# Kernel optimization log

Measured on AMD Instinct MI355X. Metric: run time of the kernel, lower is better.

## Reference

```python
import math
import jax, jax.numpy as jnp
import numpy as np

DIM_IN = 2048
DIM_OUT = 2048
BLOCK = 128
N_BLOCKS = 256
SPARSITY = 0.1
BATCH = 8192


def setup_inputs() -> dict:
    key = jax.random.key(0)
    k1, k2, k3, k4, k5 = jax.random.split(key, 5)
    x = jax.random.normal(k1, (BATCH, DIM_IN), dtype=jnp.float32)
    weight = jax.random.normal(k2, (DIM_IN, DIM_OUT), dtype=jnp.float32) * (1.0 / math.sqrt(DIM_IN))
    bias = jax.random.normal(k3, (DIM_OUT,), dtype=jnp.float32) * 0.01
    gate_w = jax.random.normal(k4, (DIM_IN, N_BLOCKS), dtype=jnp.float32) * (1.0 / math.sqrt(DIM_IN))
    gate_b = jax.random.normal(k5, (N_BLOCKS,), dtype=jnp.float32) * 0.01
    return {"x": x, "weight": weight, "bias": bias, "gate_w": gate_w, "gate_b": gate_b}


def _sparsify1d(g):
    # k-th largest kept per row; threshold, mask, renormalize (Sparsify1D)
    n = g.shape[-1]
    k = int(math.ceil(SPARSITY * n))
    topval = jax.lax.top_k(g, k)[0][:, -1:]          # (B, 1) k-th largest value
    res = jnp.where(g >= topval, g, jnp.zeros_like(g))
    return res / (jnp.sum(res, axis=-1, keepdims=True) / n)


def reference(x, weight, bias, gate_w, gate_b):
    B = x.shape[0]
    s = DIM_IN // BLOCK                               # 16 block-rows/cols
    # gate network: Linear -> Sparsify1D
    g = _sparsify1d(x @ gate_w + gate_b)              # (B, s*s)
    gb = g.reshape(B, s, s)                           # (B, s_in, s_out)
    xb = x.reshape(B, s, BLOCK)                       # (B, s_in, block)
    Wb = weight.reshape(s, BLOCK, s, BLOCK)           # (s_in, block, s_out, block)
    # gated block matrix-vector multiply:
    # y[b,q,n] = sum_{p,m} g[b,p,q] * x[b,p,m] * W[p,m,q,n]
    y = jnp.einsum('bpq,bpm,pmqn->bqn', gb, xb, Wb)
    return y.reshape(B, DIM_OUT) + bias
```

## Files before the change

### kernel.cpp

```cpp
#include <hip/hip_runtime.h>
#include <hip/hip_bf16.h>
#include <stdint.h>

#define BATCH  8192
#define DIN    2048
#define DOUT   2048
#define NB     256
#define KSEL   26
#define GDELTA 1e-4f

typedef __attribute__((ext_vector_type(2))) float f32x2;
typedef __attribute__((ext_vector_type(4))) float f32x4;
typedef __attribute__((ext_vector_type(16))) float f32x16;
typedef __attribute__((ext_vector_type(8))) __bf16 bf16x8;
typedef __attribute__((ext_vector_type(8))) unsigned short u16x8;
typedef __attribute__((ext_vector_type(4))) unsigned short u16x4;

__device__ __forceinline__ float bf2f(unsigned short u){
  union { unsigned int i; float f; } v; v.i = ((unsigned int)u) << 16; return v.f;
}
__device__ __forceinline__ unsigned short f2bf(float f){
  union { float f; unsigned int i; } v; v.f = f;
  unsigned int x = v.i;
  return (unsigned short)((x + 0x7FFFu + ((x >> 16) & 1u)) >> 16);
}
__device__ __forceinline__ unsigned short f2bf_c(float f){
  __bf16 b = (__bf16)f;
  union { __bf16 b; unsigned short u; } v; v.b = b; return v.u;
}

__global__ __launch_bounds__(256) void conv_wt(const float* __restrict__ w, unsigned short* __restrict__ wt)
{
  __shared__ float tl[64][65];
  const int k0 = blockIdx.x * 64;
  const int n0 = blockIdx.y * 64;
  const int c  = threadIdx.x & 63;
  const int r4 = threadIdx.x >> 6;
  #pragma unroll
  for (int i = 0; i < 16; i++){
    const int r = r4 * 16 + i;
    tl[r][c] = w[(size_t)(k0 + r) * DOUT + n0 + c];
  }
  __syncthreads();
  #pragma unroll
  for (int i = 0; i < 16; i++){
    const int n = r4 * 16 + i;
    wt[(size_t)(n0 + n) * DIN + k0 + c] = f2bf(tl[c][n]);
  }
}

__global__ __launch_bounds__(256) void conv_gwt(const float* __restrict__ gw,
    unsigned short* __restrict__ ghiT, unsigned short* __restrict__ gloT)
{
  __shared__ float tl[64][65];
  const int k0 = blockIdx.x * 64;
  const int n0 = blockIdx.y * 64;
  const int c  = threadIdx.x & 63;
  const int r4 = threadIdx.x >> 6;
  #pragma unroll
  for (int i = 0; i < 16; i++){
    const int r = r4 * 16 + i;
    tl[r][c] = gw[(size_t)(k0 + r) * NB + n0 + c];
  }
  __syncthreads();
  #pragma unroll
  for (int i = 0; i < 16; i++){
    const int n = r4 * 16 + i;
    const float v = tl[c][n];
    const unsigned short h = f2bf_c(v);
    ghiT[(size_t)(n0 + n) * DIN + k0 + c] = h;
    gloT[(size_t)(n0 + n) * DIN + k0 + c] = f2bf_c(v - bf2f(h));
  }
}

__global__ __launch_bounds__(256) void gate_mfma(
    const float* __restrict__ x,
    const unsigned short* __restrict__ ghiT,
    const unsigned short* __restrict__ gloT,
    float* __restrict__ part,
    unsigned short* __restrict__ xb)
{
  __shared__ unsigned short Ah[2][32][40], Al[2][32][40];
  __shared__ unsigned short Bh[2][256][40], Bl[2][256][40];

  const int b0   = blockIdx.x * 32;
  const int t    = threadIdx.x;
  const int lane = t & 63;
  const int wv   = t >> 6;
  const int l31  = lane & 31;
  const int lk   = (lane >> 5) * 8;

  const int sr = t >> 3;
  const int sk = (t & 7) * 4;
  const int bc = t >> 2;
  const int bk = (t & 3) * 8;

  f32x16 acc[2];
  acc[0] = (f32x16)0.f; acc[1] = (f32x16)0.f;

  auto STAGE = [&](int bb, int k0){
    f32x4 a = *(const f32x4*)&x[(size_t)(b0 + sr) * DIN + k0 + sk];
    u16x4 hi4, lo4;
    #pragma unroll
    for (int j = 0; j < 4; j++){
      const unsigned short h = f2bf_c(a[j]);
      hi4[j] = h;
      lo4[j] = f2bf_c(a[j] - bf2f(h));
    }
    *(u16x4*)&Ah[bb][sr][sk] = hi4;
    *(u16x4*)&Al[bb][sr][sk] = lo4;
    *(u16x4*)&xb[(size_t)(b0 + sr) * DIN + k0 + sk] = hi4;
    #pragma unroll
    for (int p = 0; p < 4; p++){
      const int col = bc + p * 64;
      u16x8 vh = *(const u16x8*)&ghiT[(size_t)col * DIN + k0 + bk];
      *(u16x8*)&Bh[bb][col][bk] = vh;
      u16x8 vl = *(const u16x8*)&gloT[(size_t)col * DIN + k0 + bk];
      *(u16x8*)&Bl[bb][col][bk] = vl;
    }
  };

  STAGE(0, 0);
  __syncthreads();
  int cur = 0;
  for (int ks = 0; ks < 64; ks++){
    if (ks < 63) STAGE(cur ^ 1, (ks + 1) * 32);
    bf16x8 ah[2], al[2], bh[2][2], bl[2][2];
    #pragma unroll
    for (int kh = 0; kh < 2; kh++){
      const int ko = kh * 16 + lk;
      ah[kh] = *(const bf16x8*)&Ah[cur][l31][ko];
      al[kh] = *(const bf16x8*)&Al[cur][l31][ko];
      #pragma unroll
      for (int n = 0; n < 2; n++){
        bh[n][kh] = *(const bf16x8*)&Bh[cur][wv * 64 + n * 32 + l31][ko];
        bl[n][kh] = *(const bf16x8*)&Bl[cur][wv * 64 + n * 32 + l31][ko];
      }
    }
    #pragma unroll
    for (int n = 0; n < 2; n++)
      #pragma unroll
      for (int kh = 0; kh < 2; kh++){
        acc[n] = __builtin_amdgcn_mfma_f32_32x32x16_bf16(ah[kh], bh[n][kh], acc[n], 0, 0, 0);
        acc[n] = __builtin_amdgcn_mfma_f32_32x32x16_bf16(ah[kh], bl[n][kh], acc[n], 0, 0, 0);
        acc[n] = __builtin_amdgcn_mfma_f32_32x32x16_bf16(al[kh], bh[n][kh], acc[n], 0, 0, 0);
      }
    __syncthreads();
    cur ^= 1;
  }

  #pragma unroll
  for (int n = 0; n < 2; n++){
    const int col = wv * 64 + n * 32 + l31;
    #pragma unroll
    for (int r = 0; r < 16; r++){
      const int row = (r & 3) + 8 * (r >> 2) + 4 * (lane >> 5);
      part[(size_t)(b0 + row) * NB + col] = acc[n][r];
    }
  }
}

__global__ __launch_bounds__(256) void topk(float* __restrict__ part,
    const float* __restrict__ gb, int* __restrict__ flags)
{
  const int lane = threadIdx.x & 63;
  const int row  = blockIdx.x * 4 + (threadIdx.x >> 6);
  f32x4* p0 = (f32x4*)&part[(size_t)row * NB];
  const f32x4* gbv = (const f32x4*)gb;
  f32x4 v = p0[lane] + gbv[lane];

  const float NEG = -3.402823466e38f;
  float w0 = v[0], w1 = v[1], w2 = v[2], w3 = v[3];
  float thr = 0.f, nxt = 0.f;
  for (int it = 0; it < KSEL + 1; it++){
    float lm = fmaxf(fmaxf(w0, w1), fmaxf(w2, w3));
    float wm = lm;
    #pragma unroll
    for (int off = 32; off; off >>= 1) wm = fmaxf(wm, __shfl_xor(wm, off, 64));
    unsigned long long ball = __ballot(lm == wm);
    int first = __ffsll(ball) - 1;
    if (lane == first){
      if      (w0 == wm) w0 = NEG;
      else if (w1 == wm) w1 = NEG;
      else if (w2 == wm) w2 = NEG;
      else               w3 = NEG;
    }
    if (it < KSEL) thr = wm; else nxt = wm;
  }
  if (lane == 0) flags[row] = (thr - nxt < GDELTA) ? 1 : 0;

  float s = 0.f;
  #pragma unroll
  for (int j = 0; j < 4; j++) s += (v[j] >= thr) ? v[j] : 0.f;
  #pragma unroll
  for (int off = 32; off; off >>= 1) s += __shfl_xor(s, off, 64);
  const float d = s * (1.0f / NB);
  f32x4 o;
  #pragma unroll
  for (int j = 0; j < 4; j++) o[j] = (v[j] >= thr) ? v[j] / d : 0.f;
  p0[lane] = o;
}

__global__ __launch_bounds__(256) void refine(
    const float* __restrict__ x, const float* __restrict__ gw,
    const float* __restrict__ gb, const int* __restrict__ flags,
    float* __restrict__ part)
{
  const int lane = threadIdx.x & 63;
  const int row  = blockIdx.x * 4 + (threadIdx.x >> 6);
  if (!flags[row]) return;

  f32x4 acc0 = (f32x4)0.f, acc1 = (f32x4)0.f;
  const float* xp = &x[(size_t)row * DIN];
  #pragma unroll 8
  for (int k = 0; k < 1024; k++){
    const float xv = xp[k];
    const f32x4 wv = *(const f32x4*)&gw[(size_t)k * NB + lane * 4];
    #pragma unroll
    for (int j = 0; j < 4; j++) acc0[j] = fmaf(xv, wv[j], acc0[j]);
  }
  #pragma unroll 8
  for (int k = 1024; k < 2048; k++){
    const float xv = xp[k];
    const f32x4 wv = *(const f32x4*)&gw[(size_t)k * NB + lane * 4];
    #pragma unroll
    for (int j = 0; j < 4; j++) acc1[j] = fmaf(xv, wv[j], acc1[j]);
  }
  const f32x4 gbv = *(const f32x4*)&gb[lane * 4];
  f32x4 v;
  #pragma unroll
  for (int j = 0; j < 4; j++) v[j] = acc0[j] + acc1[j] + gbv[j];

  const float NEG = -3.402823466e38f;
  float w0 = v[0], w1 = v[1], w2 = v[2], w3 = v[3];
  float thr = 0.f;
  for (int it = 0; it < KSEL; it++){
    float lm = fmaxf(fmaxf(w0, w1), fmaxf(w2, w3));
    float wm = lm;
    #pragma unroll
    for (int off = 32; off; off >>= 1) wm = fmaxf(wm, __shfl_xor(wm, off, 64));
    unsigned long long ball = __ballot(lm == wm);
    int first = __ffsll(ball) - 1;
    if (lane == first){
      if      (w0 == wm) w0 = NEG;
      else if (w1 == wm) w1 = NEG;
      else if (w2 == wm) w2 = NEG;
      else               w3 = NEG;
    }
    thr = wm;
  }
  float s = 0.f;
  #pragma unroll
  for (int j = 0; j < 4; j++) s += (v[j] >= thr) ? v[j] : 0.f;
  #pragma unroll
  for (int off = 32; off; off >>= 1) s += __shfl_xor(s, off, 64);
  const float d = s * (1.0f / NB);
  f32x4 o;
  #pragma unroll
  for (int j = 0; j < 4; j++) o[j] = (v[j] >= thr) ? v[j] / d : 0.f;
  *(f32x4*)&part[(size_t)row * NB + lane * 4] = o;
}

__global__ __launch_bounds__(256) void main_gemm(
    const unsigned short* __restrict__ xb,
    const unsigned short* __restrict__ wt,
    const float* __restrict__ g,
    const float* __restrict__ bias,
    float* __restrict__ out)
{
  __shared__ unsigned short xa[128][72];
  __shared__ unsigned short wb[128][72];
  __shared__ float gl[128 * 17];

  const int q    = blockIdx.x;
  const int b0   = blockIdx.y * 128;
  const int t    = threadIdx.x;
  const int lane = t & 63;
  const int wid  = t >> 6;
  const int wr   = (wid >> 1) * 64;
  const int wc   = (wid & 1) * 64;
  const int l15  = lane & 15;
  const int l4   = lane >> 4;

  for (int e = t; e < 128 * 16; e += 256){
    const int r = e >> 4, p = e & 15;
    gl[r * 17 + p] = g[(size_t)(b0 + r) * NB + p * 16 + q];
  }

  f32x4 acc[4][4];
  #pragma unroll
  for (int m = 0; m < 4; m++)
    #pragma unroll
    for (int n = 0; n < 4; n++) acc[m][n] = (f32x4)0.0f;

  const int row_s = t >> 1;
  const int half  = t & 1;

  for (int kp = 0; kp < 32; kp++){
    const int p = kp >> 1;
    __syncthreads();
    {
      const float gate = gl[row_s * 17 + p];
      const unsigned short* src = &xb[(size_t)(b0 + row_s) * DIN + kp * 64 + half * 32];
      unsigned short* dst = &xa[row_s][half * 32];
      #pragma unroll
      for (int c = 0; c < 4; c++){
        u16x8 u = *(const u16x8*)(src + c * 8);
        u16x8 o;
        #pragma unroll
        for (int j = 0; j < 8; j++) o[j] = f2bf_c(bf2f(u[j]) * gate);
        *(u16x8*)(dst + c * 8) = o;
      }
    }
    {
      const unsigned short* src = &wt[(size_t)(q * 128 + row_s) * DIN + kp * 64 + half * 32];
      unsigned short* dst = &wb[row_s][half * 32];
      #pragma unroll
      for (int c = 0; c < 4; c++)
        *(u16x8*)(dst + c * 8) = *(const u16x8*)(src + c * 8);
    }
    __syncthreads();
    #pragma unroll
    for (int ksi = 0; ksi < 2; ksi++){
      const int kk = ksi * 32 + l4 * 8;
      bf16x8 a[4], b[4];
      #pragma unroll
      for (int m = 0; m < 4; m++)
        a[m] = *(const bf16x8*)&xa[wr + m * 16 + l15][kk];
      #pragma unroll
      for (int n = 0; n < 4; n++)
        b[n] = *(const bf16x8*)&wb[wc + n * 16 + l15][kk];
      #pragma unroll
      for (int m = 0; m < 4; m++)
        #pragma unroll
        for (int n = 0; n < 4; n++)
          acc[m][n] = __builtin_amdgcn_mfma_f32_16x16x32_bf16(a[m], b[n], acc[m][n], 0, 0, 0);
    }
  }

  #pragma unroll
  for (int n = 0; n < 4; n++){
    const int col = q * 128 + wc + n * 16 + l15;
    const float bv = bias[col];
    #pragma unroll
    for (int m = 0; m < 4; m++){
      #pragma unroll
      for (int r = 0; r < 4; r++){
        const int row = b0 + wr + m * 16 + l4 * 4 + r;
        out[(size_t)row * DOUT + col] = acc[m][n][r] + bv;
      }
    }
  }
}

extern "C" void kernel_launch(void* const* d_in, const int* in_sizes, int n_in,
                              void* d_out, int out_size, void* d_ws, size_t ws_size,
                              hipStream_t stream)
{
  const float* x    = (const float*)d_in[0];
  const float* w    = (const float*)d_in[1];
  const float* bias = (const float*)d_in[2];
  const float* gw   = (const float*)d_in[3];
  const float* gb   = (const float*)d_in[4];
  float* out = (float*)d_out;

  char* wsb = (char*)d_ws;
  float*          part = (float*)wsb;
  unsigned short* wtb  = (unsigned short*)(wsb + (size_t)8  * 1024 * 1024);
  unsigned short* xbb  = (unsigned short*)(wsb + (size_t)16 * 1024 * 1024);
  unsigned short* ghiT = (unsigned short*)(wsb + (size_t)48 * 1024 * 1024);
  unsigned short* gloT = (unsigned short*)(wsb + (size_t)49 * 1024 * 1024);
  int*            flg  = (int*)           (wsb + (size_t)50 * 1024 * 1024);

  conv_wt  <<<dim3(DIN / 64, DOUT / 64), 256, 0, stream>>>(w, wtb);
  conv_gwt <<<dim3(DIN / 64, NB / 64),   256, 0, stream>>>(gw, ghiT, gloT);
  gate_mfma<<<BATCH / 32, 256, 0, stream>>>(x, ghiT, gloT, part, xbb);
  topk     <<<BATCH / 4, 256, 0, stream>>>(part, gb, flg);
  refine   <<<BATCH / 4, 256, 0, stream>>>(x, gw, gb, flg, part);
  main_gemm<<<dim3(16, BATCH / 128), 256, 0, stream>>>(xbb, wtb, part, bias, out);
}
```

Measured before the change: 305.5 us.

## Restructure gate GEMM with split-K, transposed tiling and register-loaded x

Rewrites the gate GEMM so that gate weights become the LDS-staged A operand and x is loaded straight into registers and split into hi/lo bf16 there. The reduction over K is split four ways across grid z, and topk sums the four partial results. The bf16 copy of x is no longer written, so main_gemm reads fp32 x and converts it after gating. This aims for more parallelism and less LDS and global traffic in the gate stage, at the cost of extra partial-buffer writes and the main GEMM reading twice as many bytes of x. Scaling fp32 x by the gate before rounding also changes the numerics slightly.

```diff
diff --git a/kernel.cpp b/kernel.cpp
--- a/kernel.cpp
+++ b/kernel.cpp
@@ -73,91 +73,117 @@
   }
 }
 
-__global__ __launch_bounds__(256) void gate_mfma(
+__global__ __launch_bounds__(256) void gate_flip(
     const float* __restrict__ x,
     const unsigned short* __restrict__ ghiT,
     const unsigned short* __restrict__ gloT,
-    float* __restrict__ part,
-    unsigned short* __restrict__ xb)
-{
-  __shared__ unsigned short Ah[2][32][40], Al[2][32][40];
-  __shared__ unsigned short Bh[2][256][40], Bl[2][256][40];
-
-  const int b0   = blockIdx.x * 32;
+    float* __restrict__ part)
+{
+  __shared__ unsigned short Ah[2][64][40], Al[2][64][40];
+
+  const int c0   = blockIdx.x * 64;
+  const int b0   = blockIdx.y * 256;
+  const int ks   = blockIdx.z;
+  const int k0   = ks * 512;
   const int t    = threadIdx.x;
   const int lane = t & 63;
   const int wv   = t >> 6;
   const int l31  = lane & 31;
   const int lk   = (lane >> 5) * 8;
 
-  const int sr = t >> 3;
-  const int sk = (t & 7) * 4;
-  const int bc = t >> 2;
-  const int bk = (t & 3) * 8;
-
-  f32x16 acc[2];
-  acc[0] = (f32x16)0.f; acc[1] = (f32x16)0.f;
-
-  auto STAGE = [&](int bb, int k0){
-    f32x4 a = *(const f32x4*)&x[(size_t)(b0 + sr) * DIN + k0 + sk];
-    u16x4 hi4, lo4;
-    #pragma unroll
-    for (int j = 0; j < 4; j++){
-      const unsigned short h = f2bf_c(a[j]);
-      hi4[j] = h;
-      lo4[j] = f2bf_c(a[j] - bf2f(h));
-    }
-    *(u16x4*)&Ah[bb][sr][sk] = hi4;
-    *(u16x4*)&Al[bb][sr][sk] = lo4;
-    *(u16x4*)&xb[(size_t)(b0 + sr) * DIN + k0 + sk] = hi4;
-    #pragma unroll
-    for (int p = 0; p < 4; p++){
-      const int col = bc + p * 64;
-      u16x8 vh = *(const u16x8*)&ghiT[(size_t)col * DIN + k0 + bk];
-      *(u16x8*)&Bh[bb][col][bk] = vh;
-      u16x8 vl = *(const u16x8*)&gloT[(size_t)col * DIN + k0 + bk];
-      *(u16x8*)&Bl[bb][col][bk] = vl;
-    }
+  const int sc = t >> 2;
+  const int sk = (t & 3) * 8;
+
+  f32x16 acc[2][2];
+  #pragma unroll
+  for (int m = 0; m < 2; m++)
+    #pragma unroll
+    for (int n = 0; n < 2; n++) acc[m][n] = (f32x16)0.f;
+
+  auto STAGE = [&](int bb, int kc){
+    *(u16x8*)&Ah[bb][sc][sk] = *(const u16x8*)&ghiT[(size_t)(c0 + sc) * DIN + kc + sk];
+    *(u16x8*)&Al[bb][sc][sk] = *(const u16x8*)&gloT[(size_t)(c0 + sc) * DIN + kc + sk];
   };
 
-  STAGE(0, 0);
-  __syncthreads();
-  int cur = 0;
-  for (int ks = 0; ks < 64; ks++){
-    if (ks < 63) STAGE(cur ^ 1, (ks + 1) * 32);
-    bf16x8 ah[2], al[2], bh[2][2], bl[2][2];
+  auto LOADB = [&](f32x4 (&xr)[2][2][2], int kc){
+    #pragma unroll
+    for (int n = 0; n < 2; n++){
+      const size_t rowb = (size_t)(b0 + wv * 64 + n * 32 + l31) * DIN;
+      #pragma unroll
+      for (int kh = 0; kh < 2; kh++){
+        const float* xp = &x[rowb + kc + kh * 16 + lk];
+        xr[n][kh][0] = *(const f32x4*)xp;
+        xr[n][kh][1] = *(const f32x4*)(xp + 4);
+      }
+    }
+  };
+
+  auto COMP = [&](const f32x4 (&xr)[2][2][2], int bb){
+    bf16x8 bhf[2][2], blf[2][2];
+    #pragma unroll
+    for (int n = 0; n < 2; n++)
+      #pragma unroll
+      for (int kh = 0; kh < 2; kh++){
+        bf16x8 h, l;
+        #pragma unroll
+        for (int q = 0; q < 2; q++)
+          #pragma unroll
+          for (int j = 0; j < 4; j++){
+            const float v = xr[n][kh][q][j];
+            const __bf16 hb = (__bf16)v;
+            h[q * 4 + j] = hb;
+            l[q * 4 + j] = (__bf16)(v - (float)hb);
+          }
+        bhf[n][kh] = h; blf[n][kh] = l;
+      }
     #pragma unroll
     for (int kh = 0; kh < 2; kh++){
       const int ko = kh * 16 + lk;
-      ah[kh] = *(const bf16x8*)&Ah[cur][l31][ko];
-      al[kh] = *(const bf16x8*)&Al[cur][l31][ko];
-      #pragma unroll
-      for (int n = 0; n < 2; n++){
-        bh[n][kh] = *(const bf16x8*)&Bh[cur][wv * 64 + n * 32 + l31][ko];
-        bl[n][kh] = *(const bf16x8*)&Bl[cur][wv * 64 + n * 32 + l31][ko];
-      }
-    }
-    #pragma unroll
-    for (int n = 0; n < 2; n++)
-      #pragma unroll
-      for (int kh = 0; kh < 2; kh++){
-        acc[n] = __builtin_amdgcn_mfma_f32_32x32x16_bf16(ah[kh], bh[n][kh], acc[n], 0, 0, 0);
-        acc[n] = __builtin_amdgcn_mfma_f32_32x32x16_bf16(ah[kh], bl[n][kh], acc[n], 0, 0, 0);
-        acc[n] = __builtin_amdgcn_mfma_f32_32x32x16_bf16(al[kh], bh[n][kh], acc[n], 0, 0, 0);
-      }
+      #pragma unroll
+      for (int m = 0; m < 2; m++){
+        const bf16x8 ah = *(const bf16x8*)&Ah[bb][m * 32 + l31][ko];
+        const bf16x8 al = *(const bf16x8*)&Al[bb][m * 32 + l31][ko];
+        #pragma unroll
+        for (int n = 0; n < 2; n++){
+          acc[m][n] = __builtin_amdgcn_mfma_f32_32x32x16_bf16(ah, bhf[n][kh], acc[m][n], 0, 0, 0);
+          acc[m][n] = __builtin_amdgcn_mfma_f32_32x32x16_bf16(al, bhf[n][kh], acc[m][n], 0, 0, 0);
+          acc[m][n] = __builtin_amdgcn_mfma_f32_32x32x16_bf16(ah, blf[n][kh], acc[m][n], 0, 0, 0);
+        }
+      }
+    }
+  };
+
+  f32x4 xrA[2][2][2], xrB[2][2][2];
+  LOADB(xrA, k0);
+  STAGE(0, k0);
+  __syncthreads();
+  #pragma unroll 1
+  for (int it = 0; it < 8; it++){
+    const int kc = k0 + it * 64;
+    LOADB(xrB, kc + 32);
+    STAGE(1, kc + 32);
+    COMP(xrA, 0);
     __syncthreads();
-    cur ^= 1;
-  }
-
-  #pragma unroll
-  for (int n = 0; n < 2; n++){
-    const int col = wv * 64 + n * 32 + l31;
-    #pragma unroll
-    for (int r = 0; r < 16; r++){
-      const int row = (r & 3) + 8 * (r >> 2) + 4 * (lane >> 5);
-      part[(size_t)(b0 + row) * NB + col] = acc[n][r];
-    }
-  }
+    if (it < 7){
+      LOADB(xrA, kc + 64);
+      STAGE(0, kc + 64);
+    }
+    COMP(xrB, 1);
+    __syncthreads();
+  }
+
+  float* dst = part + (size_t)ks * BATCH * NB;
+  #pragma unroll
+  for (int m = 0; m < 2; m++)
+    #pragma unroll
+    for (int n = 0; n < 2; n++){
+      const int brow = b0 + wv * 64 + n * 32 + l31;
+      #pragma unroll
+      for (int r = 0; r < 16; r++){
+        const int ccol = c0 + m * 32 + (r & 3) + 8 * (r >> 2) + 4 * (lane >> 5);
+        dst[(size_t)brow * NB + ccol] = acc[m][n][r];
+      }
+    }
 }
 
 __global__ __launch_bounds__(256) void topk(float* __restrict__ part,
@@ -166,8 +192,11 @@
   const int lane = threadIdx.x & 63;
   const int row  = blockIdx.x * 4 + (threadIdx.x >> 6);
   f32x4* p0 = (f32x4*)&part[(size_t)row * NB];
+  const f32x4* p1 = (const f32x4*)&part[(size_t)(BATCH + row) * NB];
+  const f32x4* p2 = (const f32x4*)&part[(size_t)(2 * BATCH + row) * NB];
+  const f32x4* p3 = (const f32x4*)&part[(size_t)(3 * BATCH + row) * NB];
   const f32x4* gbv = (const f32x4*)gb;
-  f32x4 v = p0[lane] + gbv[lane];
+  f32x4 v = ((p0[lane] + p1[lane]) + p2[lane]) + p3[lane] + gbv[lane];
 
   const float NEG = -3.402823466e38f;
   float w0 = v[0], w1 = v[1], w2 = v[2], w3 = v[3];
@@ -262,7 +291,7 @@
 }
 
 __global__ __launch_bounds__(256) void main_gemm(
-    const unsigned short* __restrict__ xb,
+    const float* __restrict__ x,
     const unsigned short* __restrict__ wt,
     const float* __restrict__ g,
     const float* __restrict__ bias,
@@ -301,14 +330,18 @@
     __syncthreads();
     {
       const float gate = gl[row_s * 17 + p];
-      const unsigned short* src = &xb[(size_t)(b0 + row_s) * DIN + kp * 64 + half * 32];
+      const float* src = &x[(size_t)(b0 + row_s) * DIN + kp * 64 + half * 32];
       unsigned short* dst = &xa[row_s][half * 32];
       #pragma unroll
       for (int c = 0; c < 4; c++){
-        u16x8 u = *(const u16x8*)(src + c * 8);
+        f32x4 a0 = *(const f32x4*)(src + c * 8);
+        f32x4 a1 = *(const f32x4*)(src + c * 8 + 4);
         u16x8 o;
         #pragma unroll
-        for (int j = 0; j < 8; j++) o[j] = f2bf_c(bf2f(u[j]) * gate);
+        for (int j = 0; j < 4; j++){
+          o[j]     = f2bf_c(a0[j] * gate);
+          o[4 + j] = f2bf_c(a1[j] * gate);
+        }
         *(u16x8*)(dst + c * 8) = o;
       }
     }
@@ -366,16 +399,15 @@
 
   char* wsb = (char*)d_ws;
   float*          part = (float*)wsb;
-  unsigned short* wtb  = (unsigned short*)(wsb + (size_t)8  * 1024 * 1024);
-  unsigned short* xbb  = (unsigned short*)(wsb + (size_t)16 * 1024 * 1024);
-  unsigned short* ghiT = (unsigned short*)(wsb + (size_t)48 * 1024 * 1024);
-  unsigned short* gloT = (unsigned short*)(wsb + (size_t)49 * 1024 * 1024);
-  int*            flg  = (int*)           (wsb + (size_t)50 * 1024 * 1024);
+  unsigned short* wtb  = (unsigned short*)(wsb + (size_t)32 * 1024 * 1024);
+  unsigned short* ghiT = (unsigned short*)(wsb + (size_t)40 * 1024 * 1024);
+  unsigned short* gloT = (unsigned short*)(wsb + (size_t)41 * 1024 * 1024);
+  int*            flg  = (int*)           (wsb + (size_t)42 * 1024 * 1024);
 
   conv_wt  <<<dim3(DIN / 64, DOUT / 64), 256, 0, stream>>>(w, wtb);
   conv_gwt <<<dim3(DIN / 64, NB / 64),   256, 0, stream>>>(gw, ghiT, gloT);
-  gate_mfma<<<BATCH / 32, 256, 0, stream>>>(x, ghiT, gloT, part, xbb);
+  gate_flip<<<dim3(NB / 64, BATCH / 256, 4), 256, 0, stream>>>(x, ghiT, gloT, part);
   topk     <<<BATCH / 4, 256, 0, stream>>>(part, gb, flg);
   refine   <<<BATCH / 4, 256, 0, stream>>>(x, gw, gb, flg, part);
-  main_gemm<<<dim3(16, BATCH / 128), 256, 0, stream>>>(xbb, wtb, part, bias, out);
-}
+  main_gemm<<<dim3(16, BATCH / 128), 256, 0, stream>>>(x, wtb, part, bias, out);
+}
```

After: 343.1 us. 1.12x slower.

## Split-K gate GEMM, swizzled LDS, register prefetch, and reorder main GEMM blocks

Applied to the files above, without the earlier changes.

The gate GEMM is rewritten to use 64x128 tiles with 16x16x32 MFMAs, XOR-swizzled unpadded LDS, and a split-K over two halves. It writes two partial sums that topk now adds together. The main GEMM also gets swizzled LDS, global-to-register prefetch of the next K slice that overlaps the MFMA work, and a flattened 1D grid with a remapped batch order. The weight conversion moves after refine so its buffer can reuse the gate-weight workspace. The intent is to cut LDS bank conflicts and exposed load latency and to raise gate parallelism, at the cost of extra partial-sum traffic and a tighter workspace overlap.

```diff
diff --git a/kernel.cpp b/kernel.cpp
--- a/kernel.cpp
+++ b/kernel.cpp
@@ -73,89 +73,143 @@
   }
 }
 
-__global__ __launch_bounds__(256) void gate_mfma(
+__global__ __launch_bounds__(256) void gate_v2(
     const float* __restrict__ x,
     const unsigned short* __restrict__ ghiT,
     const unsigned short* __restrict__ gloT,
     float* __restrict__ part,
     unsigned short* __restrict__ xb)
 {
-  __shared__ unsigned short Ah[2][32][40], Al[2][32][40];
-  __shared__ unsigned short Bh[2][256][40], Bl[2][256][40];
-
-  const int b0   = blockIdx.x * 32;
+  __shared__ unsigned short Axh[64][64], Axl[64][64];
+  __shared__ unsigned short Bgh[128][64], Bgl[128][64];
+
+  const int b0   = blockIdx.x * 64;
+  const int c0   = blockIdx.y * 128;
+  const int ks   = blockIdx.z;
+  const int k0   = ks * 1024;
   const int t    = threadIdx.x;
   const int lane = t & 63;
   const int wv   = t >> 6;
-  const int l31  = lane & 31;
-  const int lk   = (lane >> 5) * 8;
-
-  const int sr = t >> 3;
-  const int sk = (t & 7) * 4;
-  const int bc = t >> 2;
-  const int bk = (t & 3) * 8;
-
-  f32x16 acc[2];
-  acc[0] = (f32x16)0.f; acc[1] = (f32x16)0.f;
-
-  auto STAGE = [&](int bb, int k0){
-    f32x4 a = *(const f32x4*)&x[(size_t)(b0 + sr) * DIN + k0 + sk];
-    u16x4 hi4, lo4;
+  const int bw   = wv & 1;
+  const int cw   = wv >> 1;
+  const int l15  = lane & 15;
+  const int l4   = lane >> 4;
+  const bool emit = (blockIdx.y == 0);
+
+  const int ar = t >> 2;
+  const int ak = (t & 3) * 16;
+  const int br = t >> 1;
+  const int bk = (t & 1) * 32;
+
+  f32x4 acc[2][4];
+  #pragma unroll
+  for (int m = 0; m < 2; m++)
+    #pragma unroll
+    for (int n = 0; n < 4; n++) acc[m][n] = (f32x4)0.0f;
+
+  int aoff[2][2], boff[2][4];
+  #pragma unroll
+  for (int ksi = 0; ksi < 2; ksi++){
+    const int chunk = ksi * 4 + l4;
+    #pragma unroll
+    for (int m = 0; m < 2; m++){
+      const int row = bw * 32 + m * 16 + l15;
+      aoff[ksi][m] = row * 64 + ((chunk ^ (row & 7)) << 3);
+    }
+    #pragma unroll
+    for (int n = 0; n < 4; n++){
+      const int row = cw * 64 + n * 16 + l15;
+      boff[ksi][n] = row * 64 + ((chunk ^ (row & 7)) << 3);
+    }
+  }
+
+  f32x4 xa[4];
+  u16x8 gh[4], glo[4];
+
+  auto LOAD = [&](int kb){
+    const float* xp = &x[(size_t)(b0 + ar) * DIN + kb + ak];
+    #pragma unroll
+    for (int j = 0; j < 4; j++) xa[j] = ((const f32x4*)xp)[j];
+    const unsigned short* hp = &ghiT[(size_t)(c0 + br) * DIN + kb + bk];
+    const unsigned short* lp = &gloT[(size_t)(c0 + br) * DIN + kb + bk];
+    #pragma unroll
+    for (int j = 0; j < 4; j++){ gh[j] = ((const u16x8*)hp)[j]; glo[j] = ((const u16x8*)lp)[j]; }
+  };
+
+  auto WRITE = [&](int kb){
+    const int asw = ar & 7;
+    #pragma unroll
+    for (int h = 0; h < 2; h++){
+      u16x8 hi, lo;
+      #pragma unroll
+      for (int j = 0; j < 8; j++){
+        const float v = xa[h * 2 + (j >> 2)][j & 3];
+        const __bf16 hb = (__bf16)v;
+        union { __bf16 b; unsigned short u; } uh; uh.b = hb;
+        hi[j] = uh.u;
+        lo[j] = f2bf_c(v - (float)hb);
+      }
+      const int c8 = (((ak >> 3) + h) ^ asw) << 3;
+      *(u16x8*)&Axh[ar][c8] = hi;
+      *(u16x8*)&Axl[ar][c8] = lo;
+      if (emit) *(u16x8*)&xb[(size_t)(b0 + ar) * DIN + kb + ak + h * 8] = hi;
+    }
+    const int bsw = br & 7;
     #pragma unroll
     for (int j = 0; j < 4; j++){
-      const unsigned short h = f2bf_c(a[j]);
-      hi4[j] = h;
-      lo4[j] = f2bf_c(a[j] - bf2f(h));
-    }
-    *(u16x4*)&Ah[bb][sr][sk] = hi4;
-    *(u16x4*)&Al[bb][sr][sk] = lo4;
-    *(u16x4*)&xb[(size_t)(b0 + sr) * DIN + k0 + sk] = hi4;
-    #pragma unroll
-    for (int p = 0; p < 4; p++){
-      const int col = bc + p * 64;
-      u16x8 vh = *(const u16x8*)&ghiT[(size_t)col * DIN + k0 + bk];
-      *(u16x8*)&Bh[bb][col][bk] = vh;
-      u16x8 vl = *(const u16x8*)&gloT[(size_t)col * DIN + k0 + bk];
-      *(u16x8*)&Bl[bb][col][bk] = vl;
+      const int c8 = (((bk >> 3) + j) ^ bsw) << 3;
+      *(u16x8*)&Bgh[br][c8] = gh[j];
+      *(u16x8*)&Bgl[br][c8] = glo[j];
     }
   };
 
-  STAGE(0, 0);
-  __syncthreads();
-  int cur = 0;
-  for (int ks = 0; ks < 64; ks++){
-    if (ks < 63) STAGE(cur ^ 1, (ks + 1) * 32);
-    bf16x8 ah[2], al[2], bh[2][2], bl[2][2];
-    #pragma unroll
-    for (int kh = 0; kh < 2; kh++){
-      const int ko = kh * 16 + lk;
-      ah[kh] = *(const bf16x8*)&Ah[cur][l31][ko];
-      al[kh] = *(const bf16x8*)&Al[cur][l31][ko];
-      #pragma unroll
-      for (int n = 0; n < 2; n++){
-        bh[n][kh] = *(const bf16x8*)&Bh[cur][wv * 64 + n * 32 + l31][ko];
-        bl[n][kh] = *(const bf16x8*)&Bl[cur][wv * 64 + n * 32 + l31][ko];
+  const unsigned short* Ah0 = &Axh[0][0];
+  const unsigned short* Al0 = &Axl[0][0];
+  const unsigned short* Bh0 = &Bgh[0][0];
+  const unsigned short* Bl0 = &Bgl[0][0];
+
+  LOAD(k0);
+  #pragma unroll 1
+  for (int s = 0; s < 16; s++){
+    const int kb = k0 + s * 64;
+    __syncthreads();
+    WRITE(kb);
+    __syncthreads();
+    if (s < 15) LOAD(kb + 64);
+    #pragma unroll
+    for (int ksi = 0; ksi < 2; ksi++){
+      bf16x8 ah[2], al[2], bh[4], bl[4];
+      #pragma unroll
+      for (int m = 0; m < 2; m++){
+        ah[m] = *(const bf16x8*)&Ah0[aoff[ksi][m]];
+        al[m] = *(const bf16x8*)&Al0[aoff[ksi][m]];
       }
-    }
-    #pragma unroll
-    for (int n = 0; n < 2; n++)
-      #pragma unroll
-      for (int kh = 0; kh < 2; kh++){
-        acc[n] = __builtin_amdgcn_mfma_f32_32x32x16_bf16(ah[kh], bh[n][kh], acc[n], 0, 0, 0);
-        acc[n] = __builtin_amdgcn_mfma_f32_32x32x16_bf16(ah[kh], bl[n][kh], acc[n], 0, 0, 0);
-        acc[n] = __builtin_amdgcn_mfma_f32_32x32x16_bf16(al[kh], bh[n][kh], acc[n], 0, 0, 0);
+      #pragma unroll
+      for (int n = 0; n < 4; n++){
+        bh[n] = *(const bf16x8*)&Bh0[boff[ksi][n]];
+        bl[n] = *(const bf16x8*)&Bl0[boff[ksi][n]];
       }
-    __syncthreads();
-    cur ^= 1;
-  }
-
-  #pragma unroll
-  for (int n = 0; n < 2; n++){
-    const int col = wv * 64 + n * 32 + l31;
-    #pragma unroll
-    for (int r = 0; r < 16; r++){
-      const int row = (r & 3) + 8 * (r >> 2) + 4 * (lane >> 5);
-      part[(size_t)(b0 + row) * NB + col] = acc[n][r];
+      #pragma unroll
+      for (int m = 0; m < 2; m++)
+        #pragma unroll
+        for (int n = 0; n < 4; n++){
+          acc[m][n] = __builtin_amdgcn_mfma_f32_16x16x32_bf16(ah[m], bh[n], acc[m][n], 0, 0, 0);
+          acc[m][n] = __builtin_amdgcn_mfma_f32_16x16x32_bf16(al[m], bh[n], acc[m][n], 0, 0, 0);
+          acc[m][n] = __builtin_amdgcn_mfma_f32_16x16x32_bf16(ah[m], bl[n], acc[m][n], 0, 0, 0);
+        }
+    }
+  }
+
+  float* dst = part + (size_t)ks * BATCH * NB;
+  #pragma unroll
+  for (int m = 0; m < 2; m++){
+    const int brow = b0 + bw * 32 + m * 16 + l4 * 4;
+    #pragma unroll
+    for (int n = 0; n < 4; n++){
+      const int ccol = c0 + cw * 64 + n * 16 + l15;
+      #pragma unroll
+      for (int r = 0; r < 4; r++)
+        dst[(size_t)(brow + r) * NB + ccol] = acc[m][n][r];
     }
   }
 }
@@ -166,8 +220,9 @@
   const int lane = threadIdx.x & 63;
   const int row  = blockIdx.x * 4 + (threadIdx.x >> 6);
   f32x4* p0 = (f32x4*)&part[(size_t)row * NB];
+  const f32x4* p1 = (const f32x4*)&part[(size_t)(BATCH + row) * NB];
   const f32x4* gbv = (const f32x4*)gb;
-  f32x4 v = p0[lane] + gbv[lane];
+  f32x4 v = p0[lane] + p1[lane] + gbv[lane];
 
   const float NEG = -3.402823466e38f;
   float w0 = v[0], w1 = v[1], w2 = v[2], w3 = v[3];
@@ -261,19 +316,20 @@
   *(f32x4*)&part[(size_t)row * NB + lane * 4] = o;
 }
 
-__global__ __launch_bounds__(256) void main_gemm(
+__global__ __launch_bounds__(256) void main_v2(
     const unsigned short* __restrict__ xb,
     const unsigned short* __restrict__ wt,
     const float* __restrict__ g,
     const float* __restrict__ bias,
     float* __restrict__ out)
 {
-  __shared__ unsigned short xa[128][72];
-  __shared__ unsigned short wb[128][72];
+  __shared__ unsigned short XA[128][64];
+  __shared__ unsigned short WB[128][64];
   __shared__ float gl[128 * 17];
 
-  const int q    = blockIdx.x;
-  const int b0   = blockIdx.y * 128;
+  const int f  = blockIdx.x;
+  const int q  = f >> 6;
+  const int b0 = ((f & 7) * 8 + ((f >> 3) & 7)) * 128;
   const int t    = threadIdx.x;
   const int lane = t & 63;
   const int wid  = t >> 6;
@@ -295,41 +351,62 @@
 
   const int row_s = t >> 1;
   const int half  = t & 1;
-
+  const int kk    = half * 32;
+
+  int aoff[2][4], boff[2][4];
+  #pragma unroll
+  for (int ksi = 0; ksi < 2; ksi++){
+    const int chunk = ksi * 4 + l4;
+    #pragma unroll
+    for (int m = 0; m < 4; m++){
+      const int row = wr + m * 16 + l15;
+      aoff[ksi][m] = row * 64 + ((chunk ^ (row & 7)) << 3);
+    }
+    #pragma unroll
+    for (int n = 0; n < 4; n++){
+      const int row = wc + n * 16 + l15;
+      boff[ksi][n] = row * 64 + ((chunk ^ (row & 7)) << 3);
+    }
+  }
+
+  u16x8 ax[4], bx[4];
+  auto LOAD = [&](int kb){
+    const unsigned short* asrc = &xb[(size_t)(b0 + row_s) * DIN + kb + kk];
+    const unsigned short* bsrc = &wt[(size_t)(q * 128 + row_s) * DIN + kb + kk];
+    #pragma unroll
+    for (int j = 0; j < 4; j++){ ax[j] = ((const u16x8*)asrc)[j]; bx[j] = ((const u16x8*)bsrc)[j]; }
+  };
+  auto WRITE = [&](int p){
+    const float gate = gl[row_s * 17 + p];
+    const int sw = row_s & 7;
+    #pragma unroll
+    for (int j = 0; j < 4; j++){
+      u16x8 o;
+      #pragma unroll
+      for (int i = 0; i < 8; i++) o[i] = f2bf_c(bf2f(ax[j][i]) * gate);
+      const int c8 = ((half * 4 + j) ^ sw) << 3;
+      *(u16x8*)&XA[row_s][c8] = o;
+      *(u16x8*)&WB[row_s][c8] = bx[j];
+    }
+  };
+
+  const unsigned short* A0 = &XA[0][0];
+  const unsigned short* B0 = &WB[0][0];
+
+  LOAD(0);
+  #pragma unroll 1
   for (int kp = 0; kp < 32; kp++){
-    const int p = kp >> 1;
     __syncthreads();
-    {
-      const float gate = gl[row_s * 17 + p];
-      const unsigned short* src = &xb[(size_t)(b0 + row_s) * DIN + kp * 64 + half * 32];
-      unsigned short* dst = &xa[row_s][half * 32];
-      #pragma unroll
-      for (int c = 0; c < 4; c++){
-        u16x8 u = *(const u16x8*)(src + c * 8);
-        u16x8 o;
-        #pragma unroll
-        for (int j = 0; j < 8; j++) o[j] = f2bf_c(bf2f(u[j]) * gate);
-        *(u16x8*)(dst + c * 8) = o;
-      }
-    }
-    {
-      const unsigned short* src = &wt[(size_t)(q * 128 + row_s) * DIN + kp * 64 + half * 32];
-      unsigned short* dst = &wb[row_s][half * 32];
-      #pragma unroll
-      for (int c = 0; c < 4; c++)
-        *(u16x8*)(dst + c * 8) = *(const u16x8*)(src + c * 8);
-    }
+    WRITE(kp >> 1);
     __syncthreads();
+    if (kp < 31) LOAD((kp + 1) * 64);
     #pragma unroll
     for (int ksi = 0; ksi < 2; ksi++){
-      const int kk = ksi * 32 + l4 * 8;
       bf16x8 a[4], b[4];
       #pragma unroll
-      for (int m = 0; m < 4; m++)
-        a[m] = *(const bf16x8*)&xa[wr + m * 16 + l15][kk];
-      #pragma unroll
-      for (int n = 0; n < 4; n++)
-        b[n] = *(const bf16x8*)&wb[wc + n * 16 + l15][kk];
+      for (int m = 0; m < 4; m++) a[m] = *(const bf16x8*)&A0[aoff[ksi][m]];
+      #pragma unroll
+      for (int n = 0; n < 4; n++) b[n] = *(const bf16x8*)&B0[boff[ksi][n]];
       #pragma unroll
       for (int m = 0; m < 4; m++)
         #pragma unroll
@@ -366,16 +443,16 @@
 
   char* wsb = (char*)d_ws;
   float*          part = (float*)wsb;
-  unsigned short* wtb  = (unsigned short*)(wsb + (size_t)8  * 1024 * 1024);
   unsigned short* xbb  = (unsigned short*)(wsb + (size_t)16 * 1024 * 1024);
   unsigned short* ghiT = (unsigned short*)(wsb + (size_t)48 * 1024 * 1024);
   unsigned short* gloT = (unsigned short*)(wsb + (size_t)49 * 1024 * 1024);
   int*            flg  = (int*)           (wsb + (size_t)50 * 1024 * 1024);
-
-  conv_wt  <<<dim3(DIN / 64, DOUT / 64), 256, 0, stream>>>(w, wtb);
-  conv_gwt <<<dim3(DIN / 64, NB / 64),   256, 0, stream>>>(gw, ghiT, gloT);
-  gate_mfma<<<BATCH / 32, 256, 0, stream>>>(x, ghiT, gloT, part, xbb);
+  unsigned short* wtb  = (unsigned short*)(wsb + (size_t)48 * 1024 * 1024);
+
+  conv_gwt <<<dim3(DIN / 64, NB / 64), 256, 0, stream>>>(gw, ghiT, gloT);
+  gate_v2  <<<dim3(BATCH / 64, 2, 2), 256, 0, stream>>>(x, ghiT, gloT, part, xbb);
   topk     <<<BATCH / 4, 256, 0, stream>>>(part, gb, flg);
   refine   <<<BATCH / 4, 256, 0, stream>>>(x, gw, gb, flg, part);
-  main_gemm<<<dim3(16, BATCH / 128), 256, 0, stream>>>(xbb, wtb, part, bias, out);
-}
+  conv_wt  <<<dim3(DIN / 64, DOUT / 64), 256, 0, stream>>>(w, wtb);
+  main_v2  <<<1024, 256, 0, stream>>>(xbb, wtb, part, bias, out);
+}
```

Result: faster. 257.0 us (-15.9%).
